# Kernel optimization log

Hardware: AMD Instinct MI355X
Metric: run time of the kernel (lower is better)

## Reference

```python
import jax, jax.numpy as jnp
import numpy as np

B, S, D_IN, D_MODEL, H = 4, 2048, 1024, 1024, 16
HD = D_MODEL // H  # 64


def setup_inputs() -> dict:
    key = jax.random.key(0)
    k1, k2, k3, k4, k5 = jax.random.split(key, 5)
    x = jax.random.normal(k1, (B, S, D_IN), dtype=jnp.float32)
    mask = jnp.zeros((1, 1, S, S), dtype=jnp.float32)  # additive mask
    # qkv_layer: Linear(D_IN, 3*D_MODEL)
    W_qkv = jax.random.normal(k2, (D_IN, 3 * D_MODEL), dtype=jnp.float32) / np.sqrt(D_IN)
    b_qkv = jax.random.normal(k3, (3 * D_MODEL,), dtype=jnp.float32) * 0.01
    # linear_layer: Linear(D_MODEL, D_MODEL)
    W_o = jax.random.normal(k4, (D_MODEL, D_MODEL), dtype=jnp.float32) / np.sqrt(D_MODEL)
    b_o = jax.random.normal(k5, (D_MODEL,), dtype=jnp.float32) * 0.01
    return {"x": x, "mask": mask, "W_qkv": W_qkv, "b_qkv": b_qkv, "W_o": W_o, "b_o": b_o}


def reference(x, mask, W_qkv, b_qkv, W_o, b_o):
    b, s, _ = x.shape
    qkv = x @ W_qkv + b_qkv                                  # [B,S,3*D]
    qkv = qkv.reshape(b, s, H, 3 * HD).transpose(0, 2, 1, 3)  # [B,H,S,3*HD]
    q, k, v = jnp.split(qkv, 3, axis=-1)                     # each [B,H,S,HD]
    scale = 1.0 / jnp.sqrt(jnp.asarray(HD, dtype=q.dtype))
    scores = jnp.einsum('bhqd,bhkd->bhqk', q, k) * scale + mask  # [B,H,S,S]
    attn = jax.nn.softmax(scores, axis=-1)
    values = jnp.einsum('bhqk,bhkd->bhqd', attn, v)           # [B,H,S,HD]
    values = values.transpose(0, 2, 1, 3).reshape(b, s, H * HD)  # [B,S,D]
    out = values @ W_o + b_o
    return (out, values)
```

## Files before the change

kernel.cpp:

```cpp
#include <hip/hip_runtime.h>
#include <hip/hip_bf16.h>


typedef __attribute__((ext_vector_type(8))) short short8;
typedef __attribute__((ext_vector_type(4))) float f32x4;

#define SCL2E 0.1803368801111204f
#define L2E   1.44269504088896340736f

#define GLD16(g, l)                                                            \
  __builtin_amdgcn_global_load_lds(                                            \
      (const __attribute__((address_space(1))) unsigned int*)(g),              \
      (__attribute__((address_space(3))) unsigned int*)(l), 16, 0, 0)

__device__ __forceinline__ unsigned short f2b(float f) {
  union { float f; unsigned int u; } v; v.f = f;
  unsigned int u = v.u;
  return (unsigned short)((u + 0x7fffu + ((u >> 16) & 1u)) >> 16);
}
__device__ __forceinline__ unsigned int fbits(float f) {
  union { float f; unsigned int u; } v; v.f = f; return v.u;
}
__device__ __forceinline__ unsigned int cvt_pk_bf16(float lo, float hi) {
  unsigned int r;
  asm("v_cvt_pk_bf16_f32 %0, %1, %2" : "=v"(r) : "v"(lo), "v"(hi));
  return r;
}

__global__ void cvt_bf16(const float* __restrict__ in, ushort* __restrict__ out,
                         int n, unsigned int* __restrict__ mflags) {
  if (blockIdx.x == 0 && threadIdx.x < 16) mflags[threadIdx.x] = 0u;
  int i = (blockIdx.x * blockDim.x + threadIdx.x) * 4;
  if (i + 3 < n) {
    float4 f = *(const float4*)(in + i);
    ushort4 o;
    o.x = f2b(f.x); o.y = f2b(f.y); o.z = f2b(f.z); o.w = f2b(f.w);
    *(ushort4*)(out + i) = o;
  }
}

__global__ void mask_flags_k(const float* __restrict__ mask,
                             unsigned int* __restrict__ mflags) {
  __shared__ unsigned int s;
  const int qt = blockIdx.x >> 4, kt = blockIdx.x & 15;
  const float* base = mask + (size_t)(qt * 128) * 2048 + kt * 128;
  const int row = threadIdx.x >> 1, col0 = (threadIdx.x & 1) * 64;
  unsigned int acc = 0;
#pragma unroll
  for (int i = 0; i < 16; ++i) {
    float4 f = *(const float4*)(base + (size_t)row * 2048 + col0 + i * 4);
    acc |= fbits(f.x) | fbits(f.y) | fbits(f.z) | fbits(f.w);
  }
  acc &= 0x7fffffffu;
  if (threadIdx.x == 0) s = 0u;
  __syncthreads();
  if (acc) atomicOr(&s, 1u);
  __syncthreads();
  if (threadIdx.x == 0 && s) atomicOr(&mflags[qt], 1u << kt);
}

__global__ void transpose_cvt(const float* __restrict__ W, ushort* __restrict__ Wt,
                              int K, int N) {
  __shared__ float tile[64][65];
  int n0 = blockIdx.x * 64, k0 = blockIdx.y * 64;
  int tx = threadIdx.x & 63, ty = threadIdx.x >> 6;
#pragma unroll
  for (int i = 0; i < 64; i += 4)
    tile[ty + i][tx] = W[(size_t)(k0 + ty + i) * N + n0 + tx];
  __syncthreads();
#pragma unroll
  for (int i = 0; i < 64; i += 4)
    Wt[(size_t)(n0 + ty + i) * K + k0 + tx] = f2b(tile[tx][ty + i]);
}

template <int OUTF32, int QSCALE>
__global__ __launch_bounds__(256, 2) void gemm_bt_bias(
    const ushort* __restrict__ A, const ushort* __restrict__ Bt,
    const float* __restrict__ bias, void* __restrict__ Cout,
    int M, int N, int K) {
  __shared__ ushort As[128 * 64];
  __shared__ ushort Bs[128 * 64];
  const int lane = threadIdx.x & 63;
  const int wv = threadIdx.x >> 6;
  const int bm = blockIdx.y, bn = blockIdx.x;
  const int wm = wv >> 1, wn = wv & 1;
  f32x4 acc[4][4] = {};
  const size_t arow0 = (size_t)bm * 128;
  const size_t brow0 = (size_t)bn * 128;

  for (int k0 = 0; k0 < K; k0 += 64) {
    __syncthreads();
#pragma unroll
    for (int i = 0; i < 4; ++i) {
      int r = wv * 32 + i * 8 + (lane >> 3);
      const ushort* ga = A + (arow0 + r) * K + k0 + (lane & 7) * 8;
      GLD16(ga, As + (wv * 32 + i * 8) * 64);
      const ushort* gb = Bt + (brow0 + r) * K + k0 + (lane & 7) * 8;
      GLD16(gb, Bs + (wv * 32 + i * 8) * 64);
    }
    __syncthreads();
    short8 af[2][4], bf[2][4];
#pragma unroll
    for (int kf = 0; kf < 2; ++kf)
#pragma unroll
      for (int t = 0; t < 4; ++t) {
        af[kf][t] = *(const short8*)(As + (wm * 64 + t * 16 + (lane & 15)) * 64 +
                                     kf * 32 + (lane >> 4) * 8);
        bf[kf][t] = *(const short8*)(Bs + (wn * 64 + t * 16 + (lane & 15)) * 64 +
                                     kf * 32 + (lane >> 4) * 8);
      }
#pragma unroll
    for (int kf = 0; kf < 2; ++kf)
#pragma unroll
      for (int mt = 0; mt < 4; ++mt)
#pragma unroll
        for (int nt = 0; nt < 4; ++nt)
          acc[mt][nt] = __builtin_amdgcn_mfma_f32_16x16x32_bf16(
              af[kf][mt], bf[kf][nt], acc[mt][nt], 0, 0, 0);
  }
#pragma unroll
  for (int nt = 0; nt < 4; ++nt) {
    int col = bn * 128 + wn * 64 + nt * 16 + (lane & 15);
    float bv = bias[col];
    float scl = (QSCALE && (col % 192) < 64) ? SCL2E : 1.0f;
#pragma unroll
    for (int mt = 0; mt < 4; ++mt) {
      int row0 = bm * 128 + wm * 64 + mt * 16 + (lane >> 4) * 4;
#pragma unroll
      for (int r = 0; r < 4; ++r) {
        float v = acc[mt][nt][r] + bv;
        if (QSCALE) v *= scl;
        if (OUTF32)
          ((float*)Cout)[(size_t)(row0 + r) * N + col] = v;
        else
          ((ushort*)Cout)[(size_t)(row0 + r) * N + col] = f2b(v);
      }
    }
  }
}

__global__ __launch_bounds__(256, 2) void flash_attn(
    const ushort* __restrict__ qkv, const float* __restrict__ mask,
    const unsigned int* __restrict__ mflags,
    float* __restrict__ values_f, ushort* __restrict__ values_b) {
  __shared__ ushort Ks[2][128 * 64];
  __shared__ ushort Vt[64 * 136];

  const int lane = threadIdx.x & 63;
  const int wv = threadIdx.x >> 6;
  const int c = lane & 15;
  const int g = lane >> 4;
  const int bh = blockIdx.x & 63;
  const int qt = blockIdx.x >> 6;
  const int b = bh >> 4, h = bh & 15;
  const size_t rowbase = (size_t)b * 2048;
  const int qcol = h * 192;
  const int swz = (c & 3) << 1;
  const unsigned int flbits = mflags[qt];

  short8 qf[2][2];
#pragma unroll
  for (int mt = 0; mt < 2; ++mt)
#pragma unroll
    for (int kf = 0; kf < 2; ++kf)
      qf[mt][kf] = *(const short8*)(qkv +
          (rowbase + qt * 128 + wv * 32 + mt * 16 + c) * 3072 + qcol +
          kf * 32 + g * 8);

  f32x4 acc[2][4] = {};
  float mst[2] = {-3e38f, -3e38f}, lst[2] = {0.f, 0.f};

  const int K0 = lane * 2;
  const int dq = wv;
  const int pc0 = ((K0 >> 5) << 5) + (((K0 >> 2) & 3) << 3) +
                  (((K0 >> 4) & 1) << 2) + (K0 & 3);
  const int vdw = pc0 >> 1;
  const int gcol = (((lane & 7) ^ (((lane >> 3) & 3) << 1)) << 3);

  short8 va0, va1, vb0, vb1;

  auto loadV = [&](int t) {
    const ushort* vg = qkv + (rowbase + t * 128 + K0) * 3072 + qcol + 128 + dq * 16;
    va0 = *(const short8*)(vg);
    va1 = *(const short8*)(vg + 8);
    vb0 = *(const short8*)(vg + 3072);
    vb1 = *(const short8*)(vg + 3072 + 8);
  };
  auto writeV = [&]() {
    unsigned int* Vdw = (unsigned int*)Vt;
#pragma unroll
    for (int j = 0; j < 8; ++j)
      Vdw[(dq * 16 + j) * 68 + vdw] =
          ((unsigned int)(unsigned short)vb0[j] << 16) | (unsigned short)va0[j];
#pragma unroll
    for (int j = 0; j < 8; ++j)
      Vdw[(dq * 16 + 8 + j) * 68 + vdw] =
          ((unsigned int)(unsigned short)vb1[j] << 16) | (unsigned short)va1[j];
  };
  auto stageK = [&](int t, ushort* KsD) {
#pragma unroll
    for (int i = 0; i < 4; ++i) {
      int rloc = wv * 32 + i * 8;
      const ushort* gk = qkv + (rowbase + t * 128 + rloc + (lane >> 3)) * 3072 +
                         qcol + 64 + gcol;
      GLD16(gk, KsD + rloc * 64);
    }
  };

  const float* mrow = mask + (size_t)(qt * 128 + wv * 32 + c) * 2048 + g * 4;

  loadV(0);
  stageK(0, Ks[0]);
  writeV();

  for (int kt = 0; kt < 16; ++kt) {
    __syncthreads();
    const int cur = kt & 1;
    const ushort* KsC = Ks[cur];
    if (kt < 15) {
      loadV(kt + 1);
      stageK(kt + 1, Ks[cur ^ 1]);
    }

    const bool hasmask = (flbits >> kt) & 1u;
    const float* mkt = mrow + kt * 128;
    float4 msk0[8];
    if (hasmask) {
#pragma unroll
      for (int nt = 0; nt < 8; ++nt) msk0[nt] = *(const float4*)(mkt + nt * 16);
    }

    f32x4 sc[2][8];
    __builtin_amdgcn_s_setprio(1);
#pragma unroll
    for (int nt = 0; nt < 8; ++nt) {
      short8 k0 = *(const short8*)(KsC + (nt * 16 + c) * 64 + ((g ^ swz) << 3));
      short8 k1 = *(const short8*)(KsC + (nt * 16 + c) * 64 + (((4 + g) ^ swz) << 3));
      f32x4 z = {0.f, 0.f, 0.f, 0.f};
      sc[0][nt] = __builtin_amdgcn_mfma_f32_16x16x32_bf16(k0, qf[0][0], z, 0, 0, 0);
      sc[0][nt] = __builtin_amdgcn_mfma_f32_16x16x32_bf16(k1, qf[0][1], sc[0][nt], 0, 0, 0);
      sc[1][nt] = __builtin_amdgcn_mfma_f32_16x16x32_bf16(k0, qf[1][0], z, 0, 0, 0);
      sc[1][nt] = __builtin_amdgcn_mfma_f32_16x16x32_bf16(k1, qf[1][1], sc[1][nt], 0, 0, 0);
    }
    __builtin_amdgcn_s_setprio(0);

    __attribute__((aligned(16))) unsigned int Dw[2][16];
#pragma unroll
    for (int mt = 0; mt < 2; ++mt) {
      f32x4 t4[8];
      if (hasmask) {
#pragma unroll
        for (int nt = 0; nt < 8; ++nt) {
          float4 mk = (mt == 0) ? msk0[nt]
                                : *(const float4*)(mkt + 16 * 2048 + nt * 16);
#pragma unroll
          for (int r = 0; r < 4; ++r)
            t4[nt][r] = fmaf(((const float*)&mk)[r], L2E, sc[mt][nt][r]);
        }
      } else {
#pragma unroll
        for (int nt = 0; nt < 8; ++nt) t4[nt] = sc[mt][nt];
      }
      f32x4 vm = t4[0];
#pragma unroll
      for (int nt = 1; nt < 8; ++nt)
#pragma unroll
        for (int r = 0; r < 4; ++r) vm[r] = fmaxf(vm[r], t4[nt][r]);
      float pm = fmaxf(fmaxf(vm[0], vm[1]), fmaxf(vm[2], vm[3]));
      pm = fmaxf(pm, __shfl_xor(pm, 16));
      pm = fmaxf(pm, __shfl_xor(pm, 32));
      if (!__all(pm <= mst[mt] + 8.0f)) {
        float mnew = fmaxf(mst[mt], pm);
        float alpha = exp2f(mst[mt] - mnew);
        mst[mt] = mnew;
        lst[mt] *= alpha;
#pragma unroll
        for (int dt = 0; dt < 4; ++dt)
#pragma unroll
          for (int r = 0; r < 4; ++r) acc[mt][dt][r] *= alpha;
      }
      const float mcur = mst[mt];
      f32x4 rsv = {0.f, 0.f, 0.f, 0.f};
#pragma unroll
      for (int nt = 0; nt < 8; ++nt) {
        float p0 = exp2f(t4[nt][0] - mcur);
        float p1 = exp2f(t4[nt][1] - mcur);
        float p2 = exp2f(t4[nt][2] - mcur);
        float p3 = exp2f(t4[nt][3] - mcur);
        rsv[0] += p0; rsv[1] += p1; rsv[2] += p2; rsv[3] += p3;
        Dw[mt][nt * 2 + 0] = cvt_pk_bf16(p0, p1);
        Dw[mt][nt * 2 + 1] = cvt_pk_bf16(p2, p3);
      }
      float rs = (rsv[0] + rsv[1]) + (rsv[2] + rsv[3]);
      rs += __shfl_xor(rs, 16);
      rs += __shfl_xor(rs, 32);
      lst[mt] += rs;
    }

    const short8* bu0 = (const short8*)Dw[0];
    const short8* bu1 = (const short8*)Dw[1];
    __builtin_amdgcn_s_setprio(1);
#pragma unroll
    for (int dt = 0; dt < 4; ++dt)
#pragma unroll
      for (int kf = 0; kf < 4; ++kf) {
        short8 vf = *(const short8*)(Vt + (dt * 16 + c) * 136 + kf * 32 + g * 8);
        acc[0][dt] = __builtin_amdgcn_mfma_f32_16x16x32_bf16(vf, bu0[kf], acc[0][dt], 0, 0, 0);
        acc[1][dt] = __builtin_amdgcn_mfma_f32_16x16x32_bf16(vf, bu1[kf], acc[1][dt], 0, 0, 0);
      }
    __builtin_amdgcn_s_setprio(0);

    if (kt < 15) {
      __syncthreads();
      writeV();
    }
  }

#pragma unroll
  for (int mt = 0; mt < 2; ++mt) {
    float rl = 1.0f / lst[mt];
    size_t qrow = rowbase + qt * 128 + wv * 32 + mt * 16 + c;
#pragma unroll
    for (int dt = 0; dt < 4; ++dt) {
      int d0 = h * 64 + dt * 16 + g * 4;
      float4 o;
      o.x = acc[mt][dt][0] * rl; o.y = acc[mt][dt][1] * rl;
      o.z = acc[mt][dt][2] * rl; o.w = acc[mt][dt][3] * rl;
      *(float4*)(values_f + qrow * 1024 + d0) = o;
      ushort4 ob;
      ob.x = f2b(o.x); ob.y = f2b(o.y); ob.z = f2b(o.z); ob.w = f2b(o.w);
      *(ushort4*)(values_b + qrow * 1024 + d0) = ob;
    }
  }
}

extern "C" void kernel_launch(void* const* d_in, const int* in_sizes, int n_in,
                              void* d_out, int out_size, void* d_ws, size_t ws_size,
                              hipStream_t stream) {
  const float* x    = (const float*)d_in[0];
  const float* mask = (const float*)d_in[1];
  const float* Wqkv = (const float*)d_in[2];
  const float* bqkv = (const float*)d_in[3];
  const float* Wo   = (const float*)d_in[4];
  const float* bo   = (const float*)d_in[5];
  float* out      = (float*)d_out;
  float* values_f = out + 8388608;

  char* ws = (char*)d_ws;
  ushort* xb    = (ushort*)(ws + 0);
  ushort* wqkvt = (ushort*)(ws + 16777216);
  ushort* wot   = (ushort*)(ws + 23068672);
  ushort* qkv   = (ushort*)(ws + 25165824);
  ushort* valb  = (ushort*)(ws + 75497472);
  unsigned int* mflg = (unsigned int*)(ws + 92274688);

  cvt_bf16<<<dim3(8192), dim3(256), 0, stream>>>(x, xb, 8388608, mflg);
  mask_flags_k<<<dim3(256), dim3(256), 0, stream>>>(mask, mflg);
  transpose_cvt<<<dim3(48, 16), dim3(256), 0, stream>>>(Wqkv, wqkvt, 1024, 3072);
  transpose_cvt<<<dim3(16, 16), dim3(256), 0, stream>>>(Wo, wot, 1024, 1024);
  gemm_bt_bias<0, 1><<<dim3(24, 64), dim3(256), 0, stream>>>(
      xb, wqkvt, bqkv, (void*)qkv, 8192, 3072, 1024);
  flash_attn<<<dim3(1024), dim3(256), 0, stream>>>(qkv, mask, mflg, values_f, valb);
  gemm_bt_bias<1, 0><<<dim3(8, 64), dim3(256), 0, stream>>>(
      valb, wot, bo, (void*)out, 8192, 1024, 1024);
}
```

Baseline: 355.7 us.

## Halve attention KV tile to 64 and double-buffer transposed V in LDS

The flash attention inner loop now processes 64-key tiles over 32 iterations instead of 128-key tiles over 16. Both K and the transposed V tile are double-buffered, so the second __syncthreads per iteration is removed and the V write for the next tile overlaps with the current compute. This shrinks LDS use and register pressure (fewer score tiles and V registers per thread). In exchange there are twice as many loop iterations, each with its own barrier, max reduction and rescale check, and less MFMA work per iteration to hide latency.

```diff
diff --git a/kernel.cpp b/kernel.cpp
--- a/kernel.cpp
+++ b/kernel.cpp
@@ -143,8 +143,8 @@
     const ushort* __restrict__ qkv, const float* __restrict__ mask,
     const unsigned int* __restrict__ mflags,
     float* __restrict__ values_f, ushort* __restrict__ values_b) {
-  __shared__ ushort Ks[2][128 * 64];
-  __shared__ ushort Vt[64 * 136];
+  __shared__ ushort Ks[2][64 * 64];
+  __shared__ ushort Vt[2][64 * 80];
 
   const int lane = threadIdx.x & 63;
   const int wv = threadIdx.x >> 6;
@@ -170,38 +170,33 @@
   f32x4 acc[2][4] = {};
   float mst[2] = {-3e38f, -3e38f}, lst[2] = {0.f, 0.f};
 
-  const int K0 = lane * 2;
-  const int dq = wv;
+  const int kp = threadIdx.x & 31;
+  const int dq = threadIdx.x >> 5;
+  const int K0 = kp * 2;
   const int pc0 = ((K0 >> 5) << 5) + (((K0 >> 2) & 3) << 3) +
                   (((K0 >> 4) & 1) << 2) + (K0 & 3);
   const int vdw = pc0 >> 1;
   const int gcol = (((lane & 7) ^ (((lane >> 3) & 3) << 1)) << 3);
 
-  short8 va0, va1, vb0, vb1;
+  short8 va0, vb0;
 
   auto loadV = [&](int t) {
-    const ushort* vg = qkv + (rowbase + t * 128 + K0) * 3072 + qcol + 128 + dq * 16;
+    const ushort* vg = qkv + (rowbase + t * 64 + K0) * 3072 + qcol + 128 + dq * 8;
     va0 = *(const short8*)(vg);
-    va1 = *(const short8*)(vg + 8);
     vb0 = *(const short8*)(vg + 3072);
-    vb1 = *(const short8*)(vg + 3072 + 8);
   };
-  auto writeV = [&]() {
-    unsigned int* Vdw = (unsigned int*)Vt;
+  auto writeV = [&](ushort* dst) {
+    unsigned int* Vdw = (unsigned int*)dst;
 #pragma unroll
     for (int j = 0; j < 8; ++j)
-      Vdw[(dq * 16 + j) * 68 + vdw] =
+      Vdw[(dq * 8 + j) * 40 + vdw] =
           ((unsigned int)(unsigned short)vb0[j] << 16) | (unsigned short)va0[j];
-#pragma unroll
-    for (int j = 0; j < 8; ++j)
-      Vdw[(dq * 16 + 8 + j) * 68 + vdw] =
-          ((unsigned int)(unsigned short)vb1[j] << 16) | (unsigned short)va1[j];
   };
   auto stageK = [&](int t, ushort* KsD) {
 #pragma unroll
-    for (int i = 0; i < 4; ++i) {
-      int rloc = wv * 32 + i * 8;
-      const ushort* gk = qkv + (rowbase + t * 128 + rloc + (lane >> 3)) * 3072 +
+    for (int i = 0; i < 2; ++i) {
+      int rloc = wv * 16 + i * 8;
+      const ushort* gk = qkv + (rowbase + t * 64 + rloc + (lane >> 3)) * 3072 +
                          qcol + 64 + gcol;
       GLD16(gk, KsD + rloc * 64);
     }
@@ -211,29 +206,30 @@
 
   loadV(0);
   stageK(0, Ks[0]);
-  writeV();
-
-  for (int kt = 0; kt < 16; ++kt) {
+  writeV(Vt[0]);
+
+  for (int kt = 0; kt < 32; ++kt) {
     __syncthreads();
     const int cur = kt & 1;
     const ushort* KsC = Ks[cur];
-    if (kt < 15) {
+    const ushort* VtC = Vt[cur];
+    if (kt < 31) {
       loadV(kt + 1);
       stageK(kt + 1, Ks[cur ^ 1]);
     }
 
-    const bool hasmask = (flbits >> kt) & 1u;
-    const float* mkt = mrow + kt * 128;
-    float4 msk0[8];
+    const bool hasmask = (flbits >> (kt >> 1)) & 1u;
+    const float* mkt = mrow + kt * 64;
+    float4 msk0[4];
     if (hasmask) {
 #pragma unroll
-      for (int nt = 0; nt < 8; ++nt) msk0[nt] = *(const float4*)(mkt + nt * 16);
-    }
-
-    f32x4 sc[2][8];
+      for (int nt = 0; nt < 4; ++nt) msk0[nt] = *(const float4*)(mkt + nt * 16);
+    }
+
+    f32x4 sc[2][4];
     __builtin_amdgcn_s_setprio(1);
 #pragma unroll
-    for (int nt = 0; nt < 8; ++nt) {
+    for (int nt = 0; nt < 4; ++nt) {
       short8 k0 = *(const short8*)(KsC + (nt * 16 + c) * 64 + ((g ^ swz) << 3));
       short8 k1 = *(const short8*)(KsC + (nt * 16 + c) * 64 + (((4 + g) ^ swz) << 3));
       f32x4 z = {0.f, 0.f, 0.f, 0.f};
@@ -244,13 +240,13 @@
     }
     __builtin_amdgcn_s_setprio(0);
 
-    __attribute__((aligned(16))) unsigned int Dw[2][16];
+    __attribute__((aligned(16))) unsigned int Dw[2][8];
 #pragma unroll
     for (int mt = 0; mt < 2; ++mt) {
-      f32x4 t4[8];
+      f32x4 t4[4];
       if (hasmask) {
 #pragma unroll
-        for (int nt = 0; nt < 8; ++nt) {
+        for (int nt = 0; nt < 4; ++nt) {
           float4 mk = (mt == 0) ? msk0[nt]
                                 : *(const float4*)(mkt + 16 * 2048 + nt * 16);
 #pragma unroll
@@ -259,13 +255,12 @@
         }
       } else {
 #pragma unroll
-        for (int nt = 0; nt < 8; ++nt) t4[nt] = sc[mt][nt];
-      }
-      f32x4 vm = t4[0];
-#pragma unroll
-      for (int nt = 1; nt < 8; ++nt)
-#pragma unroll
-        for (int r = 0; r < 4; ++r) vm[r] = fmaxf(vm[r], t4[nt][r]);
+        for (int nt = 0; nt < 4; ++nt) t4[nt] = sc[mt][nt];
+      }
+      f32x4 vm;
+#pragma unroll
+      for (int r = 0; r < 4; ++r)
+        vm[r] = fmaxf(fmaxf(t4[0][r], t4[1][r]), fmaxf(t4[2][r], t4[3][r]));
       float pm = fmaxf(fmaxf(vm[0], vm[1]), fmaxf(vm[2], vm[3]));
       pm = fmaxf(pm, __shfl_xor(pm, 16));
       pm = fmaxf(pm, __shfl_xor(pm, 32));
@@ -282,7 +277,7 @@
       const float mcur = mst[mt];
       f32x4 rsv = {0.f, 0.f, 0.f, 0.f};
 #pragma unroll
-      for (int nt = 0; nt < 8; ++nt) {
+      for (int nt = 0; nt < 4; ++nt) {
         float p0 = exp2f(t4[nt][0] - mcur);
         float p1 = exp2f(t4[nt][1] - mcur);
         float p2 = exp2f(t4[nt][2] - mcur);
@@ -303,17 +298,14 @@
 #pragma unroll
     for (int dt = 0; dt < 4; ++dt)
 #pragma unroll
-      for (int kf = 0; kf < 4; ++kf) {
-        short8 vf = *(const short8*)(Vt + (dt * 16 + c) * 136 + kf * 32 + g * 8);
+      for (int kf = 0; kf < 2; ++kf) {
+        short8 vf = *(const short8*)(VtC + (dt * 16 + c) * 80 + kf * 32 + g * 8);
         acc[0][dt] = __builtin_amdgcn_mfma_f32_16x16x32_bf16(vf, bu0[kf], acc[0][dt], 0, 0, 0);
         acc[1][dt] = __builtin_amdgcn_mfma_f32_16x16x32_bf16(vf, bu1[kf], acc[1][dt], 0, 0, 0);
       }
     __builtin_amdgcn_s_setprio(0);
 
-    if (kt < 15) {
-      __syncthreads();
-      writeV();
-    }
+    if (kt < 31) writeV(Vt[cur ^ 1]);
   }
 
 #pragma unroll
```

Result: slower. 371.4 us (+4.4%).
